# Optimization experiments

Measured on AMD Instinct MI355X. Metric: run time of the kernel, lower is better.

Reference implementation:

```python
import jax, jax.numpy as jnp
import numpy as np

E, K, H, I = 8, 2, 768, 1152  # experts, top_k, hidden, intermediate
T = 4096  # total tokens


def setup_inputs() -> dict:
    key = jax.random.key(0)
    ks = jax.random.split(key, 6)
    return {
        "x": jax.random.normal(ks[0], (T, H), jnp.float32),
        "gate_w": jax.random.normal(ks[1], (E, H), jnp.float32) * 0.02,
        "correction_bias": jnp.zeros((E,), jnp.float32),
        "Wi": jax.random.normal(ks[2], (E, H, 2 * I), jnp.float32) * 0.02,
        "Wo": jax.random.normal(ks[3], (E, I, H), jnp.float32) * 0.02,
        "shared_Wi": jax.random.normal(ks[4], (2 * I, H), jnp.float32) * 0.02,
        "shared_Wo": jax.random.normal(ks[5], (H, I), jnp.float32) * 0.02,
    }


def reference(x, gate_w, correction_bias, Wi, Wo, shared_Wi, shared_Wo):
    # ---- shared SwiGLU expert (dropout=0 in eval) ----
    sh = x @ shared_Wi.T                      # (T, 2I)
    s_in, s_gate = sh[:, :I], sh[:, I:]
    shared_out = (jax.nn.silu(s_in) * s_gate) @ shared_Wo.T  # (T, H)

    # ---- sigmoid top-k router with bias correction ----
    logits = jax.nn.sigmoid(x @ gate_w.T)     # (T, E)
    sel = logits + correction_bias
    _, indices = jax.lax.top_k(sel, K)        # (T, K)
    weights = jnp.take_along_axis(logits, indices, axis=-1)  # bias-free scores
    weights = weights / jnp.sum(weights, axis=-1, keepdims=True)

    # combine weight per (expert, token): cw[e, t] = sum_k weights[t,k]*[indices[t,k]==e]
    one_hot = jax.nn.one_hot(indices, E, dtype=x.dtype)      # (T, K, E)
    cw = jnp.einsum("tke,tk->et", one_hot, weights)          # (E, T)

    # ---- experts: SwiGLU per expert, weighted scatter-combine ----
    h = jnp.einsum("th,ehf->etf", x, Wi)      # (E, T, 2I)
    proj, gate = h[..., :I], h[..., I:]
    act = jax.nn.silu(gate) * proj            # (E, T, I)
    act = act * cw[:, :, None]                # fold combine weights before Wo
    expert_out = jnp.einsum("eti,eih->th", act, Wo)          # (T, H)

    return expert_out + shared_out
```

## Files before the change

### kernel.cpp

```cpp
#include <hip/hip_runtime.h>
#include <stdint.h>

#define E_  8
#define H_  768
#define I_  1152
#define T_  4096
#define F2_ (2*I_)

typedef unsigned short u16;
typedef __attribute__((ext_vector_type(8))) __bf16 bf16x8;
typedef __attribute__((ext_vector_type(4))) float floatx4;

typedef const void __attribute__((address_space(1))) as1_void;
typedef void __attribute__((address_space(3))) as3_void;

__device__ __forceinline__ void gld16(void* lds, const void* g) {
  __builtin_amdgcn_global_load_lds((as1_void*)g, (as3_void*)lds, 16, 0, 0);
}

__device__ __forceinline__ u16 f2bf(float f) {
  union { float f; unsigned int i; } v; v.f = f;
  unsigned int r = v.i + 0x7FFF + ((v.i >> 16) & 1);
  return (u16)(r >> 16);
}

__global__ void convert_two(const float* __restrict__ s1, u16* __restrict__ d1, int n1,
                            const float* __restrict__ s2, u16* __restrict__ d2) {
  int i = (blockIdx.x * 256 + threadIdx.x) * 4;
  const float* s; u16* d;
  if (i < n1) { s = s1 + i; d = d1 + i; }
  else        { s = s2 + (i - n1); d = d2 + (i - n1); }
  float4 v = *(const float4*)s;
  ushort4 u;
  u.x = f2bf(v.x); u.y = f2bf(v.y); u.z = f2bf(v.z); u.w = f2bf(v.w);
  *(ushort4*)d = u;
}

__global__ void transpose_f2b(const float* __restrict__ src, u16* __restrict__ dst,
                              int R, int C) {
  __shared__ u16 tile[64][65];
  const float* s = src + (long)blockIdx.z * R * C;
  u16*         d = dst + (long)blockIdx.z * R * C;
  int r0 = blockIdx.y * 64, c0 = blockIdx.x * 64;
  int tx = threadIdx.x, ty = threadIdx.y;
  #pragma unroll
  for (int k = 0; k < 64; k += 8)
    tile[ty + k][tx] = f2bf(s[(long)(r0 + ty + k) * C + (c0 + tx)]);
  __syncthreads();
  #pragma unroll
  for (int k = 0; k < 64; k += 8)
    d[(long)(c0 + ty + k) * R + (r0 + tx)] = tile[tx][ty + k];
}

__global__ void gate_kernel(const float* __restrict__ x, const float* __restrict__ gw,
                            const float* __restrict__ bias,
                            int* __restrict__ top2e, float* __restrict__ top2w,
                            u16* __restrict__ xb) {
  int t    = blockIdx.x * 4 + (threadIdx.x >> 6);
  int lane = threadIdx.x & 63;
  float acc[E_];
  #pragma unroll
  for (int e = 0; e < E_; e++) acc[e] = 0.f;
  #pragma unroll
  for (int i = 0; i < H_ / 256; i++) {
    int c = i * 256 + lane * 4;
    float4 xv = *(const float4*)(x + (long)t * H_ + c);
    ushort4 u;
    u.x = f2bf(xv.x); u.y = f2bf(xv.y); u.z = f2bf(xv.z); u.w = f2bf(xv.w);
    *(ushort4*)(xb + (long)t * H_ + c) = u;
    #pragma unroll
    for (int e = 0; e < E_; e++) {
      float4 g = *(const float4*)(gw + e * H_ + c);
      acc[e] += xv.x * g.x + xv.y * g.y + xv.z * g.z + xv.w * g.w;
    }
  }
  #pragma unroll
  for (int e = 0; e < E_; e++) {
    #pragma unroll
    for (int s = 32; s > 0; s >>= 1) acc[e] += __shfl_xor(acc[e], s);
  }
  if (lane == 0) {
    float logits[E_], sel[E_];
    #pragma unroll
    for (int e = 0; e < E_; e++) {
      logits[e] = 1.f / (1.f + expf(-acc[e]));
      sel[e]    = logits[e] + bias[e];
    }
    int i0 = 0;
    #pragma unroll
    for (int e = 1; e < E_; e++) if (sel[e] > sel[i0]) i0 = e;
    int i1 = (i0 == 0) ? 1 : 0;
    #pragma unroll
    for (int e = 0; e < E_; e++) if (e != i0 && sel[e] > sel[i1]) i1 = e;
    float w0 = logits[i0], w1 = logits[i1], s = w0 + w1;
    top2e[t * 2 + 0] = i0;  top2w[t * 2 + 0] = w0 / s;
    top2e[t * 2 + 1] = i1;  top2w[t * 2 + 1] = w1 / s;
  }
}

__global__ void build_lists(const int* __restrict__ top2e, const float* __restrict__ top2w,
                            int* __restrict__ counts, int* __restrict__ offs,
                            int* __restrict__ list, float* __restrict__ wlist,
                            int* __restrict__ pos) {
  __shared__ int scnt[4][E_];
  __shared__ int sq[4];
  __shared__ int soffs[E_];
  int e = blockIdx.x;
  int tid = threadIdx.x, w = tid >> 6, lane = tid & 63;
  const int Q = (2 * T_) / 4;

  int c8[E_];
  #pragma unroll
  for (int q = 0; q < E_; q++) c8[q] = 0;
  for (int i = tid; i < 2 * T_; i += 256) {
    int v = top2e[i];
    #pragma unroll
    for (int q = 0; q < E_; q++) c8[q] += (v == q);
  }
  int qstart = w * Q;
  int ce = 0;
  for (int i = qstart + lane; i < qstart + Q; i += 64) ce += (top2e[i] == e);
  #pragma unroll
  for (int q = 0; q < E_; q++)
    #pragma unroll
    for (int s = 32; s > 0; s >>= 1) c8[q] += __shfl_xor(c8[q], s);
  #pragma unroll
  for (int s = 32; s > 0; s >>= 1) ce += __shfl_xor(ce, s);
  if (lane == 0) {
    #pragma unroll
    for (int q = 0; q < E_; q++) scnt[w][q] = c8[q];
    sq[w] = ce;
  }
  __syncthreads();
  if (tid == 0) {
    int s = 0;
    #pragma unroll
    for (int q = 0; q < E_; q++) {
      int tot = scnt[0][q] + scnt[1][q] + scnt[2][q] + scnt[3][q];
      soffs[q] = s;
      if (e == 0) { counts[q] = tot; offs[q] = s; }
      s += tot;
    }
    if (e == 0) { counts[8] = T_; offs[8] = 2 * T_; }
  }
  __syncthreads();
  int base = soffs[e];
  #pragma unroll
  for (int w2 = 0; w2 < 4; w2++) if (w2 < w) base += sq[w2];
  unsigned long long lt = (lane == 63) ? (~0ull >> 1) : ((1ull << lane) - 1);
  for (int i0 = qstart; i0 < qstart + Q; i0 += 64) {
    int s = i0 + lane;
    bool m = (top2e[s] == e);
    unsigned long long mask = __ballot(m);
    if (m) {
      int p = base + __popcll(mask & lt);
      list[p]  = s >> 1;
      wlist[p] = top2w[s];
      pos[s]   = p;
    }
    base += __popcll(mask);
  }
  for (int t = e * (T_ / 8) + tid; t < (e + 1) * (T_ / 8); t += 256) {
    list[2 * T_ + t]  = t;
    wlist[2 * T_ + t] = 1.f;
  }
}

#define PP1 168
__global__ __launch_bounds__(256, 2)
void gemm_act_all(const u16* __restrict__ A, const u16* __restrict__ WiT,
                  const u16* __restrict__ sWib, u16* __restrict__ act,
                  const int* __restrict__ list, const float* __restrict__ wlist,
                  const int* __restrict__ counts, const int* __restrict__ offsets) {
  __shared__ __align__(16) u16 As[128 * 64];
  __shared__ __align__(16) u16 Bs[2][64 * 64];

  int id = blockIdx.x;
  int y  = id / PP1, p = id - y * PP1;
  if (p >= 162) return;
  int z = p / 18, xblk = p - z * 18;

  int cnt = counts[z], off = offsets[z];
  int row0 = y * 128;
  if (row0 >= cnt) return;
  const u16* B = (z == 8) ? sWib : (WiT + (long)z * F2_ * H_);
  int n0 = xblk * 64;

  int tid  = threadIdx.x;
  int lane = tid & 63, wv = tid >> 6;
  int wr   = wv >> 1, wc = wv & 1;
  int half = lane & 15, quad = lane >> 4;

  int rA  = tid >> 3;
  int lc8 = ((tid & 7) ^ (rA & 7)) * 8;
  const u16* ap[4];
  #pragma unroll
  for (int n = 0; n < 4; n++) {
    int rr = min(row0 + rA + n * 32, cnt - 1);
    ap[n] = A + (long)list[off + rr] * H_ + lc8;
  }
  const u16* bp[2][2];
  #pragma unroll
  for (int h = 0; h < 2; h++)
    #pragma unroll
    for (int m = 0; m < 2; m++)
      bp[h][m] = B + (long)(h * I_ + n0 + m * 32 + rA) * H_ + lc8;

  floatx4 acc[2][4][2];
  #pragma unroll
  for (int q = 0; q < 2; q++)
    #pragma unroll
    for (int i = 0; i < 4; i++)
      #pragma unroll
      for (int j = 0; j < 2; j++) acc[q][i][j] = (floatx4)0.f;

  for (int k0 = 0; k0 < H_; k0 += 64) {
    if (k0) __syncthreads();
    #pragma unroll
    for (int n = 0; n < 4; n++) gld16(As + (n * 256 + tid) * 8, ap[n] + k0);
    #pragma unroll
    for (int h = 0; h < 2; h++)
      #pragma unroll
      for (int m = 0; m < 2; m++) gld16(Bs[h] + (m * 256 + tid) * 8, bp[h][m] + k0);
    __syncthreads();
    #pragma unroll
    for (int kk = 0; kk < 2; kk++) {
      int cs = ((kk * 4 + quad) ^ (half & 7)) * 8;
      bf16x8 a[4], bq[2][2];
      #pragma unroll
      for (int i = 0; i < 4; i++)
        a[i] = *(const bf16x8*)(As + (wr * 64 + i * 16 + half) * 64 + cs);
      #pragma unroll
      for (int q = 0; q < 2; q++)
        #pragma unroll
        for (int j = 0; j < 2; j++)
          bq[q][j] = *(const bf16x8*)(Bs[q] + (wc * 32 + j * 16 + half) * 64 + cs);
      #pragma unroll
      for (int i = 0; i < 4; i++)
        #pragma unroll
        for (int q = 0; q < 2; q++)
          #pragma unroll
          for (int j = 0; j < 2; j++)
            acc[q][i][j] = __builtin_amdgcn_mfma_f32_16x16x32_bf16(a[i], bq[q][j], acc[q][i][j], 0, 0, 0);
    }
  }

  bool sh = (z == 8);
  #pragma unroll
  for (int i = 0; i < 4; i++) {
    #pragma unroll
    for (int r = 0; r < 4; r++) {
      int g = row0 + wr * 64 + i * 16 + quad * 4 + r;
      if (g < cnt) {
        float w = wlist[off + g];
        #pragma unroll
        for (int j = 0; j < 2; j++) {
          float va = acc[0][i][j][r];
          float vb = acc[1][i][j][r];
          float zz = sh ? va : vb;
          float o  = sh ? vb : va;
          float sg = zz / (1.f + expf(-zz));
          float v  = sg * o * w;
          int col  = n0 + wc * 32 + j * 16 + half;
          act[(long)(off + g) * I_ + col] = f2bf(v);
        }
      }
    }
  }
}

#define PP2 56
__global__ __launch_bounds__(256, 2)
void gemm_out_all(const u16* __restrict__ A, const u16* __restrict__ WoT,
                  const u16* __restrict__ sWob, float* __restrict__ out,
                  float* __restrict__ eobuf,
                  const int* __restrict__ counts, const int* __restrict__ offsets) {
  __shared__ __align__(16) u16 As[128 * 64];
  __shared__ __align__(16) u16 Bs[128 * 64];

  int id = blockIdx.x;
  int y  = id / PP2, p = id - y * PP2;
  if (p >= 54) return;
  int z = p / 6, xblk = p - z * 6;

  int cnt = counts[z], off = offsets[z];
  int row0 = y * 128;
  if (row0 >= cnt) return;
  const u16* B = (z == 8) ? sWob : (WoT + (long)z * H_ * I_);
  int n0 = xblk * 128;

  int tid  = threadIdx.x;
  int lane = tid & 63, wv = tid >> 6;
  int wr   = wv >> 1, wc = wv & 1;
  int half = lane & 15, quad = lane >> 4;

  int rA  = tid >> 3;
  int lc8 = ((tid & 7) ^ (rA & 7)) * 8;
  const u16* ap[4];
  #pragma unroll
  for (int n = 0; n < 4; n++) {
    long rr = off + min(row0 + rA + n * 32, cnt - 1);
    ap[n] = A + rr * I_ + lc8;
  }
  const u16* bp[4];
  #pragma unroll
  for (int m = 0; m < 4; m++)
    bp[m] = B + (long)(n0 + m * 32 + rA) * I_ + lc8;

  floatx4 acc[4][4];
  #pragma unroll
  for (int i = 0; i < 4; i++)
    #pragma unroll
    for (int j = 0; j < 4; j++) acc[i][j] = (floatx4)0.f;

  for (int k0 = 0; k0 < I_; k0 += 64) {
    if (k0) __syncthreads();
    #pragma unroll
    for (int n = 0; n < 4; n++) gld16(As + (n * 256 + tid) * 8, ap[n] + k0);
    #pragma unroll
    for (int m = 0; m < 4; m++) gld16(Bs + (m * 256 + tid) * 8, bp[m] + k0);
    __syncthreads();
    #pragma unroll
    for (int kk = 0; kk < 2; kk++) {
      int cs = ((kk * 4 + quad) ^ (half & 7)) * 8;
      bf16x8 a[4], b[4];
      #pragma unroll
      for (int i = 0; i < 4; i++)
        a[i] = *(const bf16x8*)(As + (wr * 64 + i * 16 + half) * 64 + cs);
      #pragma unroll
      for (int j = 0; j < 4; j++)
        b[j] = *(const bf16x8*)(Bs + (wc * 64 + j * 16 + half) * 64 + cs);
      #pragma unroll
      for (int i = 0; i < 4; i++)
        #pragma unroll
        for (int j = 0; j < 4; j++)
          acc[i][j] = __builtin_amdgcn_mfma_f32_16x16x32_bf16(a[i], b[j], acc[i][j], 0, 0, 0);
    }
  }

  bool sh = (z == 8);
  #pragma unroll
  for (int i = 0; i < 4; i++) {
    #pragma unroll
    for (int r = 0; r < 4; r++) {
      int g = row0 + wr * 64 + i * 16 + quad * 4 + r;
      if (g < cnt) {
        float* orow = sh ? (out + (long)g * H_) : (eobuf + (long)(off + g) * H_);
        #pragma unroll
        for (int j = 0; j < 4; j++) {
          int col = n0 + wc * 64 + j * 16 + half;
          orow[col] = acc[i][j][r];
        }
      }
    }
  }
}

__global__ void final_reduce(float* __restrict__ out, const float* __restrict__ eobuf,
                             const int* __restrict__ pos) {
  int gid = blockIdx.x * 256 + threadIdx.x;
  int t = gid / (H_ / 4), c = (gid % (H_ / 4)) * 4;
  int p0 = pos[t * 2], p1 = pos[t * 2 + 1];
  float4 a = *(const float4*)(out   + (long)t  * H_ + c);
  float4 b = *(const float4*)(eobuf + (long)p0 * H_ + c);
  float4 d = *(const float4*)(eobuf + (long)p1 * H_ + c);
  a.x += b.x + d.x; a.y += b.y + d.y; a.z += b.z + d.z; a.w += b.w + d.w;
  *(float4*)(out + (long)t * H_ + c) = a;
}

extern "C" void kernel_launch(void* const* d_in, const int* in_sizes, int n_in,
                              void* d_out, int out_size, void* d_ws, size_t ws_size,
                              hipStream_t stream) {
  const float* x      = (const float*)d_in[0];
  const float* gate_w = (const float*)d_in[1];
  const float* bias   = (const float*)d_in[2];
  const float* Wi     = (const float*)d_in[3];
  const float* Wo     = (const float*)d_in[4];
  const float* sWi    = (const float*)d_in[5];
  const float* sWo    = (const float*)d_in[6];
  float* out          = (float*)d_out;

  char* ws = (char*)d_ws;
  size_t o = 0;
  auto alloc = [&](size_t bytes) -> void* {
    o = (o + 255) & ~(size_t)255;
    void* p = ws + o;
    o += bytes;
    return p;
  };
  u16*   xb    = (u16*)  alloc((size_t)T_ * H_ * 2);
  u16*   sWib  = (u16*)  alloc((size_t)F2_ * H_ * 2);
  u16*   sWob  = (u16*)  alloc((size_t)H_ * I_ * 2);
  u16*   WiT   = (u16*)  alloc((size_t)E_ * F2_ * H_ * 2);
  u16*   WoT   = (u16*)  alloc((size_t)E_ * H_ * I_ * 2);
  u16*   act   = (u16*)  alloc((size_t)3 * T_ * I_ * 2);
  int*   top2e = (int*)  alloc((size_t)T_ * 2 * 4);
  float* top2w = (float*)alloc((size_t)T_ * 2 * 4);
  int*   count = (int*)  alloc(9 * 4);
  int*   offs  = (int*)  alloc(9 * 4);
  int*   list  = (int*)  alloc((size_t)3 * T_ * 4);
  float* wlist = (float*)alloc((size_t)3 * T_ * 4);
  int*   pos   = (int*)  alloc((size_t)2 * T_ * 4);
  float* eobuf = (float*)WiT;

  gate_kernel<<<T_ / 4, 256, 0, stream>>>(x, gate_w, bias, top2e, top2w, xb);
  build_lists<<<E_, 256, 0, stream>>>(top2e, top2w, count, offs, list, wlist, pos);

  convert_two<<<(F2_ * H_ + H_ * I_) / 1024, 256, 0, stream>>>(
      sWi, sWib, F2_ * H_, sWo, sWob);
  transpose_f2b<<<dim3(F2_ / 64, H_ / 64, E_), dim3(64, 8), 0, stream>>>(Wi, WiT, H_, F2_);
  transpose_f2b<<<dim3(H_ / 64, I_ / 64, E_), dim3(64, 8), 0, stream>>>(Wo, WoT, I_, H_);

  gemm_act_all<<<32 * PP1, 256, 0, stream>>>(xb, WiT, sWib, act, list, wlist, count, offs);
  gemm_out_all<<<32 * PP2, 256, 0, stream>>>(act, WoT, sWob, out, eobuf, count, offs);
  final_reduce<<<(T_ * (H_ / 4)) / 256, 256, 0, stream>>>(out, eobuf, pos);
}
```

Baseline: 294.5 us.

## Fuse prep kernels, compact GEMM grids by row-block prefix, load B from global

```diff
diff --git a/kernel.cpp b/kernel.cpp
--- a/kernel.cpp
+++ b/kernel.cpp
@@ -6,6 +6,7 @@
 #define I_  1152
 #define T_  4096
 #define F2_ (2*I_)
+#define RBMAX 104
 
 typedef unsigned short u16;
 typedef __attribute__((ext_vector_type(8))) __bf16 bf16x8;
@@ -24,84 +25,99 @@
   return (u16)(r >> 16);
 }
 
-__global__ void convert_two(const float* __restrict__ s1, u16* __restrict__ d1, int n1,
-                            const float* __restrict__ s2, u16* __restrict__ d2) {
-  int i = (blockIdx.x * 256 + threadIdx.x) * 4;
-  const float* s; u16* d;
-  if (i < n1) { s = s1 + i; d = d1 + i; }
-  else        { s = s2 + (i - n1); d = d2 + (i - n1); }
-  float4 v = *(const float4*)s;
-  ushort4 u;
-  u.x = f2bf(v.x); u.y = f2bf(v.y); u.z = f2bf(v.z); u.w = f2bf(v.w);
-  *(ushort4*)d = u;
-}
-
-__global__ void transpose_f2b(const float* __restrict__ src, u16* __restrict__ dst,
-                              int R, int C) {
-  __shared__ u16 tile[64][65];
-  const float* s = src + (long)blockIdx.z * R * C;
-  u16*         d = dst + (long)blockIdx.z * R * C;
-  int r0 = blockIdx.y * 64, c0 = blockIdx.x * 64;
-  int tx = threadIdx.x, ty = threadIdx.y;
-  #pragma unroll
-  for (int k = 0; k < 64; k += 8)
+__device__ __forceinline__ void transpose_tile(const float* __restrict__ s,
+                                               u16* __restrict__ d, int R, int C,
+                                               int r0, int c0, u16 (*tile)[65], int tid) {
+  int tx = tid & 63, ty = tid >> 6;
+  #pragma unroll
+  for (int k = 0; k < 64; k += 4)
     tile[ty + k][tx] = f2bf(s[(long)(r0 + ty + k) * C + (c0 + tx)]);
   __syncthreads();
   #pragma unroll
-  for (int k = 0; k < 64; k += 8)
+  for (int k = 0; k < 64; k += 4)
     d[(long)(c0 + ty + k) * R + (r0 + tx)] = tile[tx][ty + k];
 }
 
-__global__ void gate_kernel(const float* __restrict__ x, const float* __restrict__ gw,
+__global__ void prep_kernel(const float* __restrict__ x, const float* __restrict__ gw,
                             const float* __restrict__ bias,
                             int* __restrict__ top2e, float* __restrict__ top2w,
-                            u16* __restrict__ xb) {
-  int t    = blockIdx.x * 4 + (threadIdx.x >> 6);
-  int lane = threadIdx.x & 63;
-  float acc[E_];
-  #pragma unroll
-  for (int e = 0; e < E_; e++) acc[e] = 0.f;
-  #pragma unroll
-  for (int i = 0; i < H_ / 256; i++) {
-    int c = i * 256 + lane * 4;
-    float4 xv = *(const float4*)(x + (long)t * H_ + c);
+                            u16* __restrict__ xb,
+                            const float* __restrict__ sWi, u16* __restrict__ sWib,
+                            const float* __restrict__ sWo, u16* __restrict__ sWob,
+                            const float* __restrict__ Wi, u16* __restrict__ WiT,
+                            const float* __restrict__ Wo, u16* __restrict__ WoT) {
+  __shared__ u16 tile[64][65];
+  int b = blockIdx.x, tid = threadIdx.x;
+  if (b < 1024) {
+    int t    = b * 4 + (tid >> 6);
+    int lane = tid & 63;
+    float acc[E_];
+    #pragma unroll
+    for (int e = 0; e < E_; e++) acc[e] = 0.f;
+    #pragma unroll
+    for (int i = 0; i < H_ / 256; i++) {
+      int c = i * 256 + lane * 4;
+      float4 xv = *(const float4*)(x + (long)t * H_ + c);
+      ushort4 u;
+      u.x = f2bf(xv.x); u.y = f2bf(xv.y); u.z = f2bf(xv.z); u.w = f2bf(xv.w);
+      *(ushort4*)(xb + (long)t * H_ + c) = u;
+      #pragma unroll
+      for (int e = 0; e < E_; e++) {
+        float4 g = *(const float4*)(gw + e * H_ + c);
+        acc[e] += xv.x * g.x + xv.y * g.y + xv.z * g.z + xv.w * g.w;
+      }
+    }
+    #pragma unroll
+    for (int e = 0; e < E_; e++) {
+      #pragma unroll
+      for (int s = 32; s > 0; s >>= 1) acc[e] += __shfl_xor(acc[e], s);
+    }
+    if (lane == 0) {
+      float logits[E_], sel[E_];
+      #pragma unroll
+      for (int e = 0; e < E_; e++) {
+        logits[e] = 1.f / (1.f + expf(-acc[e]));
+        sel[e]    = logits[e] + bias[e];
+      }
+      int i0 = 0;
+      #pragma unroll
+      for (int e = 1; e < E_; e++) if (sel[e] > sel[i0]) i0 = e;
+      int i1 = (i0 == 0) ? 1 : 0;
+      #pragma unroll
+      for (int e = 0; e < E_; e++) if (e != i0 && sel[e] > sel[i1]) i1 = e;
+      float w0 = logits[i0], w1 = logits[i1], s = w0 + w1;
+      top2e[t * 2 + 0] = i0;  top2w[t * 2 + 0] = w0 / s;
+      top2e[t * 2 + 1] = i1;  top2w[t * 2 + 1] = w1 / s;
+    }
+  } else if (b < 3616) {
+    int i = (b - 1024) * 1024 + tid * 4;
+    const int n1 = F2_ * H_;
+    const float* s; u16* d;
+    if (i < n1) { s = sWi + i; d = sWib + i; }
+    else        { s = sWo + (i - n1); d = sWob + (i - n1); }
+    float4 v = *(const float4*)s;
     ushort4 u;
-    u.x = f2bf(xv.x); u.y = f2bf(xv.y); u.z = f2bf(xv.z); u.w = f2bf(xv.w);
-    *(ushort4*)(xb + (long)t * H_ + c) = u;
-    #pragma unroll
-    for (int e = 0; e < E_; e++) {
-      float4 g = *(const float4*)(gw + e * H_ + c);
-      acc[e] += xv.x * g.x + xv.y * g.y + xv.z * g.z + xv.w * g.w;
-    }
-  }
-  #pragma unroll
-  for (int e = 0; e < E_; e++) {
-    #pragma unroll
-    for (int s = 32; s > 0; s >>= 1) acc[e] += __shfl_xor(acc[e], s);
-  }
-  if (lane == 0) {
-    float logits[E_], sel[E_];
-    #pragma unroll
-    for (int e = 0; e < E_; e++) {
-      logits[e] = 1.f / (1.f + expf(-acc[e]));
-      sel[e]    = logits[e] + bias[e];
-    }
-    int i0 = 0;
-    #pragma unroll
-    for (int e = 1; e < E_; e++) if (sel[e] > sel[i0]) i0 = e;
-    int i1 = (i0 == 0) ? 1 : 0;
-    #pragma unroll
-    for (int e = 0; e < E_; e++) if (e != i0 && sel[e] > sel[i1]) i1 = e;
-    float w0 = logits[i0], w1 = logits[i1], s = w0 + w1;
-    top2e[t * 2 + 0] = i0;  top2w[t * 2 + 0] = w0 / s;
-    top2e[t * 2 + 1] = i1;  top2w[t * 2 + 1] = w1 / s;
+    u.x = f2bf(v.x); u.y = f2bf(v.y); u.z = f2bf(v.z); u.w = f2bf(v.w);
+    *(ushort4*)d = u;
+  } else if (b < 7072) {
+    int idx = b - 3616;
+    int bx = idx % 36, tmp = idx / 36;
+    int by = tmp % 12, bz = tmp / 12;
+    transpose_tile(Wi + (long)bz * H_ * F2_, WiT + (long)bz * F2_ * H_,
+                   H_, F2_, by * 64, bx * 64, tile, tid);
+  } else {
+    int idx = b - 7072;
+    int bx = idx % 12, tmp = idx / 12;
+    int by = tmp % 18, bz = tmp / 18;
+    transpose_tile(Wo + (long)bz * I_ * H_, WoT + (long)bz * H_ * I_,
+                   I_, H_, by * 64, bx * 64, tile, tid);
   }
 }
 
 __global__ void build_lists(const int* __restrict__ top2e, const float* __restrict__ top2w,
                             int* __restrict__ counts, int* __restrict__ offs,
                             int* __restrict__ list, float* __restrict__ wlist,
-                            int* __restrict__ pos) {
+                            int* __restrict__ pos, int* __restrict__ rbc) {
   __shared__ int scnt[4][E_];
   __shared__ int sq[4];
   __shared__ int soffs[E_];
@@ -133,15 +149,23 @@
   }
   __syncthreads();
   if (tid == 0) {
-    int s = 0;
+    int s = 0, rb = 0;
+    if (e == 0) rbc[0] = 0;
     #pragma unroll
     for (int q = 0; q < E_; q++) {
       int tot = scnt[0][q] + scnt[1][q] + scnt[2][q] + scnt[3][q];
       soffs[q] = s;
-      if (e == 0) { counts[q] = tot; offs[q] = s; }
+      if (e == 0) {
+        counts[q] = tot; offs[q] = s;
+        rb += (tot + 127) / 128;
+        rbc[q + 1] = rb;
+      }
       s += tot;
     }
-    if (e == 0) { counts[8] = T_; offs[8] = 2 * T_; }
+    if (e == 0) {
+      counts[8] = T_; offs[8] = 2 * T_;
+      rbc[9] = rb + T_ / 128;
+    }
   }
   __syncthreads();
   int base = soffs[e];
@@ -166,23 +190,23 @@
   }
 }
 
-#define PP1 168
 __global__ __launch_bounds__(256, 2)
 void gemm_act_all(const u16* __restrict__ A, const u16* __restrict__ WiT,
                   const u16* __restrict__ sWib, u16* __restrict__ act,
                   const int* __restrict__ list, const float* __restrict__ wlist,
-                  const int* __restrict__ counts, const int* __restrict__ offsets) {
+                  const int* __restrict__ counts, const int* __restrict__ offsets,
+                  const int* __restrict__ rbc) {
   __shared__ __align__(16) u16 As[128 * 64];
-  __shared__ __align__(16) u16 Bs[2][64 * 64];
 
   int id = blockIdx.x;
-  int y  = id / PP1, p = id - y * PP1;
-  if (p >= 162) return;
-  int z = p / 18, xblk = p - z * 18;
-
+  int r = id / 24, xblk = id - r * 24;
+  if (xblk >= 18) return;
+  if (r >= rbc[9]) return;
+  int z = 0;
+  while (r >= rbc[z + 1]) z++;
+  int y = r - rbc[z];
   int cnt = counts[z], off = offsets[z];
   int row0 = y * 128;
-  if (row0 >= cnt) return;
   const u16* B = (z == 8) ? sWib : (WiT + (long)z * F2_ * H_);
   int n0 = xblk * 64;
 
@@ -199,12 +223,12 @@
     int rr = min(row0 + rA + n * 32, cnt - 1);
     ap[n] = A + (long)list[off + rr] * H_ + lc8;
   }
-  const u16* bp[2][2];
+  const u16* bb[2][2];
   #pragma unroll
   for (int h = 0; h < 2; h++)
     #pragma unroll
-    for (int m = 0; m < 2; m++)
-      bp[h][m] = B + (long)(h * I_ + n0 + m * 32 + rA) * H_ + lc8;
+    for (int j = 0; j < 2; j++)
+      bb[h][j] = B + (long)(h * I_ + n0 + wc * 32 + j * 16 + half) * H_ + quad * 8;
 
   floatx4 acc[2][4][2];
   #pragma unroll
@@ -215,33 +239,32 @@
       for (int j = 0; j < 2; j++) acc[q][i][j] = (floatx4)0.f;
 
   for (int k0 = 0; k0 < H_; k0 += 64) {
+    bf16x8 bq[2][2][2];
+    #pragma unroll
+    for (int kk = 0; kk < 2; kk++)
+      #pragma unroll
+      for (int h = 0; h < 2; h++)
+        #pragma unroll
+        for (int j = 0; j < 2; j++)
+          bq[kk][h][j] = *(const bf16x8*)(bb[h][j] + k0 + kk * 32);
     if (k0) __syncthreads();
     #pragma unroll
     for (int n = 0; n < 4; n++) gld16(As + (n * 256 + tid) * 8, ap[n] + k0);
-    #pragma unroll
-    for (int h = 0; h < 2; h++)
-      #pragma unroll
-      for (int m = 0; m < 2; m++) gld16(Bs[h] + (m * 256 + tid) * 8, bp[h][m] + k0);
     __syncthreads();
     #pragma unroll
     for (int kk = 0; kk < 2; kk++) {
       int cs = ((kk * 4 + quad) ^ (half & 7)) * 8;
-      bf16x8 a[4], bq[2][2];
+      bf16x8 a[4];
       #pragma unroll
       for (int i = 0; i < 4; i++)
         a[i] = *(const bf16x8*)(As + (wr * 64 + i * 16 + half) * 64 + cs);
-      #pragma unroll
-      for (int q = 0; q < 2; q++)
-        #pragma unroll
-        for (int j = 0; j < 2; j++)
-          bq[q][j] = *(const bf16x8*)(Bs[q] + (wc * 32 + j * 16 + half) * 64 + cs);
       #pragma unroll
       for (int i = 0; i < 4; i++)
         #pragma unroll
         for (int q = 0; q < 2; q++)
           #pragma unroll
           for (int j = 0; j < 2; j++)
-            acc[q][i][j] = __builtin_amdgcn_mfma_f32_16x16x32_bf16(a[i], bq[q][j], acc[q][i][j], 0, 0, 0);
+            acc[q][i][j] = __builtin_amdgcn_mfma_f32_16x16x32_bf16(a[i], bq[kk][q][j], acc[q][i][j], 0, 0, 0);
     }
   }
 
@@ -249,14 +272,14 @@
   #pragma unroll
   for (int i = 0; i < 4; i++) {
     #pragma unroll
-    for (int r = 0; r < 4; r++) {
-      int g = row0 + wr * 64 + i * 16 + quad * 4 + r;
+    for (int rr = 0; rr < 4; rr++) {
+      int g = row0 + wr * 64 + i * 16 + quad * 4 + rr;
       if (g < cnt) {
         float w = wlist[off + g];
         #pragma unroll
         for (int j = 0; j < 2; j++) {
-          float va = acc[0][i][j][r];
-          float vb = acc[1][i][j][r];
+          float va = acc[0][i][j][rr];
+          float vb = acc[1][i][j][rr];
           float zz = sh ? va : vb;
           float o  = sh ? vb : va;
           float sg = zz / (1.f + expf(-zz));
@@ -269,23 +292,23 @@
   }
 }
 
-#define PP2 56
 __global__ __launch_bounds__(256, 2)
 void gemm_out_all(const u16* __restrict__ A, const u16* __restrict__ WoT,
                   const u16* __restrict__ sWob, float* __restrict__ out,
                   float* __restrict__ eobuf,
-                  const int* __restrict__ counts, const int* __restrict__ offsets) {
+                  const int* __restrict__ counts, const int* __restrict__ offsets,
+                  const int* __restrict__ rbc) {
   __shared__ __align__(16) u16 As[128 * 64];
-  __shared__ __align__(16) u16 Bs[128 * 64];
 
   int id = blockIdx.x;
-  int y  = id / PP2, p = id - y * PP2;
-  if (p >= 54) return;
-  int z = p / 6, xblk = p - z * 6;
-
+  int r = id >> 3, xblk = id & 7;
+  if (xblk >= 6) return;
+  if (r >= rbc[9]) return;
+  int z = 0;
+  while (r >= rbc[z + 1]) z++;
+  int y = r - rbc[z];
   int cnt = counts[z], off = offsets[z];
   int row0 = y * 128;
-  if (row0 >= cnt) return;
   const u16* B = (z == 8) ? sWob : (WoT + (long)z * H_ * I_);
   int n0 = xblk * 128;
 
@@ -302,10 +325,10 @@
     long rr = off + min(row0 + rA + n * 32, cnt - 1);
     ap[n] = A + rr * I_ + lc8;
   }
-  const u16* bp[4];
-  #pragma unroll
-  for (int m = 0; m < 4; m++)
-    bp[m] = B + (long)(n0 + m * 32 + rA) * I_ + lc8;
+  const u16* bb[4];
+  #pragma unroll
+  for (int j = 0; j < 4; j++)
+    bb[j] = B + (long)(n0 + wc * 64 + j * 16 + half) * I_ + quad * 8;
 
   floatx4 acc[4][4];
   #pragma unroll
@@ -314,27 +337,28 @@
     for (int j = 0; j < 4; j++) acc[i][j] = (floatx4)0.f;
 
   for (int k0 = 0; k0 < I_; k0 += 64) {
+    bf16x8 bq[2][4];
+    #pragma unroll
+    for (int kk = 0; kk < 2; kk++)
+      #pragma unroll
+      for (int j = 0; j < 4; j++)
+        bq[kk][j] = *(const bf16x8*)(bb[j] + k0 + kk * 32);
     if (k0) __syncthreads();
     #pragma unroll
     for (int n = 0; n < 4; n++) gld16(As + (n * 256 + tid) * 8, ap[n] + k0);
-    #pragma unroll
-    for (int m = 0; m < 4; m++) gld16(Bs + (m * 256 + tid) * 8, bp[m] + k0);
     __syncthreads();
     #pragma unroll
     for (int kk = 0; kk < 2; kk++) {
       int cs = ((kk * 4 + quad) ^ (half & 7)) * 8;
-      bf16x8 a[4], b[4];
+      bf16x8 a[4];
       #pragma unroll
       for (int i = 0; i < 4; i++)
         a[i] = *(const bf16x8*)(As + (wr * 64 + i * 16 + half) * 64 + cs);
-      #pragma unroll
-      for (int j = 0; j < 4; j++)
-        b[j] = *(const bf16x8*)(Bs + (wc * 64 + j * 16 + half) * 64 + cs);
       #pragma unroll
       for (int i = 0; i < 4; i++)
         #pragma unroll
         for (int j = 0; j < 4; j++)
-          acc[i][j] = __builtin_amdgcn_mfma_f32_16x16x32_bf16(a[i], b[j], acc[i][j], 0, 0, 0);
+          acc[i][j] = __builtin_amdgcn_mfma_f32_16x16x32_bf16(a[i], bq[kk][j], acc[i][j], 0, 0, 0);
     }
   }
 
@@ -342,14 +366,14 @@
   #pragma unroll
   for (int i = 0; i < 4; i++) {
     #pragma unroll
-    for (int r = 0; r < 4; r++) {
-      int g = row0 + wr * 64 + i * 16 + quad * 4 + r;
+    for (int rr = 0; rr < 4; rr++) {
+      int g = row0 + wr * 64 + i * 16 + quad * 4 + rr;
       if (g < cnt) {
         float* orow = sh ? (out + (long)g * H_) : (eobuf + (long)(off + g) * H_);
         #pragma unroll
         for (int j = 0; j < 4; j++) {
           int col = n0 + wc * 64 + j * 16 + half;
-          orow[col] = acc[i][j][r];
+          orow[col] = acc[i][j][rr];
         }
       }
     }
@@ -401,17 +425,16 @@
   int*   list  = (int*)  alloc((size_t)3 * T_ * 4);
   float* wlist = (float*)alloc((size_t)3 * T_ * 4);
   int*   pos   = (int*)  alloc((size_t)2 * T_ * 4);
+  int*   rbc   = (int*)  alloc(16 * 4);
   float* eobuf = (float*)WiT;
 
-  gate_kernel<<<T_ / 4, 256, 0, stream>>>(x, gate_w, bias, top2e, top2w, xb);
-  build_lists<<<E_, 256, 0, stream>>>(top2e, top2w, count, offs, list, wlist, pos);
-
-  convert_two<<<(F2_ * H_ + H_ * I_) / 1024, 256, 0, stream>>>(
-      sWi, sWib, F2_ * H_, sWo, sWob);
-  transpose_f2b<<<dim3(F2_ / 64, H_ / 64, E_), dim3(64, 8), 0, stream>>>(Wi, WiT, H_, F2_);
-  transpose_f2b<<<dim3(H_ / 64, I_ / 64, E_), dim3(64, 8), 0, stream>>>(Wo, WoT, I_, H_);
-
-  gemm_act_all<<<32 * PP1, 256, 0, stream>>>(xb, WiT, sWib, act, list, wlist, count, offs);
-  gemm_out_all<<<32 * PP2, 256, 0, stream>>>(act, WoT, sWob, out, eobuf, count, offs);
+  prep_kernel<<<8800, 256, 0, stream>>>(x, gate_w, bias, top2e, top2w, xb,
+                                        sWi, sWib, sWo, sWob, Wi, WiT, Wo, WoT);
+  build_lists<<<E_, 256, 0, stream>>>(top2e, top2w, count, offs, list, wlist, pos, rbc);
+
+  gemm_act_all<<<RBMAX * 24, 256, 0, stream>>>(xb, WiT, sWib, act, list, wlist,
+                                               count, offs, rbc);
+  gemm_out_all<<<RBMAX * 8, 256, 0, stream>>>(act, WoT, sWob, out, eobuf,
+                                              count, offs, rbc);
   final_reduce<<<(T_ * (H_ / 4)) / 256, 256, 0, stream>>>(out, eobuf, pos);
 }
```

Result: slower. 406.1 us (+37.9%).
